# Kernel tuning notes

Measured on AMD Instinct MI355X. Metric: run time of the kernel, lower is better.

## Reference

```python
import jax, jax.numpy as jnp
import numpy as np

B, C, H = 8, 512, 2048
GROUPS = 32
EPS = 1e-6


def setup_inputs() -> dict:
    key = jax.random.key(0)
    ks = jax.random.split(key, 10)
    s = 1.0 / np.sqrt(C)
    return {
        "x": jax.random.normal(ks[0], (B, C, H), dtype=jnp.float32),
        "gamma": jnp.ones((C,), jnp.float32),
        "beta": jnp.zeros((C,), jnp.float32),
        "wq": jax.random.normal(ks[1], (C, C), jnp.float32) * s,
        "bq": jnp.zeros((C,), jnp.float32),
        "wk": jax.random.normal(ks[2], (C, C), jnp.float32) * s,
        "bk": jnp.zeros((C,), jnp.float32),
        "wv": jax.random.normal(ks[3], (C, C), jnp.float32) * s,
        "bv": jnp.zeros((C,), jnp.float32),
        "wp": jax.random.normal(ks[4], (C, C), jnp.float32) * s,
        "bp": jnp.zeros((C,), jnp.float32),
    }


def group_norm(x, gamma, beta):
    b, c, h = x.shape
    xr = x.reshape(b, GROUPS, c // GROUPS, h)
    mean = xr.mean(axis=(2, 3), keepdims=True)
    var = xr.var(axis=(2, 3), keepdims=True)
    xn = ((xr - mean) * jax.lax.rsqrt(var + EPS)).reshape(b, c, h)
    return xn * gamma[None, :, None] + beta[None, :, None]


def conv1x1(x, w, b):
    # 1x1 Conv1d == channel-mixing GEMM: [C_out,C_in] x [b,C_in,h]
    return jnp.einsum("oc,bch->boh", w, x) + b[None, :, None]


def reference(x, gamma, beta, wq, bq, wk, bk, wv, bv, wp, bp):
    b, c, h = x.shape
    hn = group_norm(x, gamma, beta)
    q = conv1x1(hn, wq, bq)  # [b,c,h]
    k = conv1x1(hn, wk, bk)
    v = conv1x1(hn, wv, bv)
    # scores w[b,i,j] = sum_c q[b,c,i] k[b,c,j] / sqrt(c)
    w = jnp.einsum("bci,bcj->bij", q, k) * (c ** -0.5)
    w = jax.nn.softmax(w, axis=2)
    # h_[b,c,i] = sum_j v[b,c,j] w[b,i,j]
    h_ = jnp.einsum("bcj,bij->bci", v, w)
    out = conv1x1(h_, wp, bp)
    return x + out
```

## Files before the change

### kernel.cpp

```cpp
#include <hip/hip_runtime.h>
#include <stdint.h>

typedef unsigned short u16;
typedef short s16x8 __attribute__((ext_vector_type(8)));
typedef float f32x4 __attribute__((ext_vector_type(4)));

#define BM 128
#define BN 128
#define BK 32
#define KPAD 40

#define WAITV(n) asm volatile("s_waitcnt vmcnt(" #n ")" ::: "memory")
#define BARR()   asm volatile("s_barrier" ::: "memory")
#define SB0()    __builtin_amdgcn_sched_barrier(0)

__device__ __forceinline__ float bf2f(u16 b) {
    union { unsigned int u; float f; } v; v.u = ((unsigned int)b) << 16; return v.f;
}
__device__ __forceinline__ u16 f2bf(float f) {
    union { float f; unsigned int u; } v; v.f = f;
    unsigned int u = v.u;
    u += 0x7fffu + ((u >> 16) & 1u);
    return (u16)(u >> 16);
}
__device__ __forceinline__ void async_cp16(const u16* g, u16* l) {
    __builtin_amdgcn_global_load_lds((const __attribute__((address_space(1))) void*)g,
                                     (__attribute__((address_space(3))) void*)l, 16, 0, 0);
}

__global__ __launch_bounds__(256) void gn_stats(const float* __restrict__ x,
                                                float* __restrict__ mean,
                                                float* __restrict__ rstd) {
    const int bg = blockIdx.x;
    const float* p = x + (long)bg * 16 * 2048;
    float s = 0.f, ss = 0.f;
    for (int it = 0; it < 32; it++) {
        const float4 v = *reinterpret_cast<const float4*>(p + ((it * 256 + threadIdx.x) << 2));
        s += v.x + v.y + v.z + v.w;
        ss += v.x * v.x + v.y * v.y + v.z * v.z + v.w * v.w;
    }
    const int lane = threadIdx.x & 63, wave = threadIdx.x >> 6;
#pragma unroll
    for (int o = 32; o > 0; o >>= 1) { s += __shfl_down(s, o, 64); ss += __shfl_down(ss, o, 64); }
    __shared__ float rb[8];
    if (lane == 0) { rb[wave] = s; rb[4 + wave] = ss; }
    __syncthreads();
    if (threadIdx.x == 0) {
        float S = rb[0] + rb[1] + rb[2] + rb[3];
        float SS = rb[4] + rb[5] + rb[6] + rb[7];
        float mu = S * (1.f / 32768.f);
        float var = SS * (1.f / 32768.f) - mu * mu;
        mean[bg] = mu;
        rstd[bg] = rsqrtf(var + 1e-6f);
    }
}

__global__ __launch_bounds__(256) void gn_apply_t(const float* __restrict__ x,
                                                  const float* __restrict__ gamma,
                                                  const float* __restrict__ beta,
                                                  const float* __restrict__ mean,
                                                  const float* __restrict__ rstd,
                                                  u16* __restrict__ hnT) {
    const int b = blockIdx.z, c0 = blockIdx.y * 64, h0 = blockIdx.x * 64;
    __shared__ __align__(16) u16 T[64][72];
    const int tid = threadIdx.x;
#pragma unroll
    for (int sidx = 0; sidx < 4; sidx++) {
        int ch = tid + sidx * 256;
        int cc = ch >> 4, h4 = (ch & 15) * 4;
        int c = c0 + cc;
        float mu = mean[b * 32 + (c >> 4)], rs = rstd[b * 32 + (c >> 4)];
        float ga = gamma[c], be = beta[c];
        const float4 v = *reinterpret_cast<const float4*>(x + ((long)b * 512 + c) * 2048 + h0 + h4);
        ushort4 pk;
        pk.x = f2bf((v.x - mu) * rs * ga + be);
        pk.y = f2bf((v.y - mu) * rs * ga + be);
        pk.z = f2bf((v.z - mu) * rs * ga + be);
        pk.w = f2bf((v.w - mu) * rs * ga + be);
        *reinterpret_cast<ushort4*>(&T[cc][h4]) = pk;
    }
    __syncthreads();
#pragma unroll
    for (int sidx = 0; sidx < 2; sidx++) {
        int ch = tid + sidx * 256;
        int hh = ch >> 3, c8 = (ch & 7) * 8;
        unsigned int o[4];
#pragma unroll
        for (int i = 0; i < 4; i++) {
            u16 lo = T[c8 + 2 * i][hh];
            u16 hi = T[c8 + 2 * i + 1][hh];
            o[i] = (unsigned int)lo | ((unsigned int)hi << 16);
        }
        *reinterpret_cast<uint4*>(hnT + ((long)b * 2048 + h0 + hh) * 512 + c0 + c8) =
            uint4{o[0], o[1], o[2], o[3]};
    }
}

__global__ __launch_bounds__(256) void w2bf(const float* __restrict__ a,
                                            const float* __restrict__ b,
                                            const float* __restrict__ c,
                                            u16* __restrict__ dst) {
    const float* s = (blockIdx.y == 0) ? a : (blockIdx.y == 1) ? b : c;
    const int i = (blockIdx.x * 256 + threadIdx.x) * 4;
    const float4 v = *reinterpret_cast<const float4*>(s + i);
    ushort4 p;
    p.x = f2bf(v.x); p.y = f2bf(v.y); p.z = f2bf(v.z); p.w = f2bf(v.w);
    *reinterpret_cast<ushort4*>(dst + (long)blockIdx.y * 262144 + i) = p;
}

__global__ __launch_bounds__(256) void softmax_rows(u16* __restrict__ S) {
    u16* p = S + (long)blockIdx.x * 2048;
    const int tid = threadIdx.x;
    uint4 v = *reinterpret_cast<const uint4*>(p + (tid << 3));
    unsigned int w[4] = {v.x, v.y, v.z, v.w};
    float f[8];
#pragma unroll
    for (int i = 0; i < 4; i++) {
        f[2 * i]     = bf2f((u16)(w[i] & 0xffffu));
        f[2 * i + 1] = bf2f((u16)(w[i] >> 16));
    }
    float m = f[0];
#pragma unroll
    for (int i = 1; i < 8; i++) m = fmaxf(m, f[i]);
    const int lane = tid & 63, wave = tid >> 6;
#pragma unroll
    for (int o = 32; o > 0; o >>= 1) m = fmaxf(m, __shfl_down(m, o, 64));
    __shared__ float rb[4];
    __shared__ float bc;
    if (lane == 0) rb[wave] = m;
    __syncthreads();
    if (tid == 0) bc = fmaxf(fmaxf(rb[0], rb[1]), fmaxf(rb[2], rb[3]));
    __syncthreads();
    m = bc;
    float s = 0.f;
#pragma unroll
    for (int i = 0; i < 8; i++) { f[i] = __expf(f[i] - m); s += f[i]; }
#pragma unroll
    for (int o = 32; o > 0; o >>= 1) s += __shfl_down(s, o, 64);
    __syncthreads();
    if (lane == 0) rb[wave] = s;
    __syncthreads();
    if (tid == 0) bc = 1.f / (rb[0] + rb[1] + rb[2] + rb[3]);
    __syncthreads();
    const float inv = bc;
#pragma unroll
    for (int i = 0; i < 4; i++)
        w[i] = (unsigned int)f2bf(f[2 * i] * inv) | ((unsigned int)f2bf(f[2 * i + 1] * inv) << 16);
    *reinterpret_cast<uint4*>(p + (tid << 3)) = uint4{w[0], w[1], w[2], w[3]};
}

__global__ __launch_bounds__(512, 1) void gemm256_s(const u16* __restrict__ Ag, long sA,
                                                    const u16* __restrict__ Bg, long sB,
                                                    u16* __restrict__ Og, long sO,
                                                    int K, int lda, int ldb, int ldo,
                                                    float scale) {
    const int bx = blockIdx.x;
    const int b = bx & 7, s = bx >> 3;
    const int ty = s & 7, tx = s >> 3;
    const int m0 = ty * 256, n0 = tx * 256;
    Ag += (long)b * sA;
    Bg += (long)b * sB;
    u16* O = Og + (long)b * sO;

    __shared__ __align__(16) u16 LA[2][2][128 * 64];
    __shared__ __align__(16) u16 LB[2][2][128 * 64];

    const int tid = threadIdx.x;
    const int lane = tid & 63, wave = tid >> 6;
    const int wm = wave >> 2, w4 = wave & 3;
    const int l15 = lane & 15, quad = lane >> 4;

    const int sw   = (l15 & 7) << 3;
    const int slt0 = ((quad << 3)) ^ sw;
    const int slt1 = (32 + (quad << 3)) ^ sw;
    const int arow_u = (wm * 64 + l15) * 64;
    const int brow_u = (w4 * 32 + l15) * 64;

    const int l8 = lane >> 3;
    const int lrow0 = wave * 8 + l8;
    const int sEl = (((lane & 7) ^ ((lane >> 3) & 7)) << 3);
    int pA[2], pB[2];
    pA[0] = (m0 + lrow0) * lda + sEl;
    pA[1] = (m0 + 64 + lrow0) * lda + sEl;
    {
        const int gb = (lrow0 >> 5) * 64 + (lrow0 & 31);
        pB[0] = (n0 + gb) * ldb + sEl;
        pB[1] = (n0 + gb + 32) * ldb + sEl;
    }
    const int jA = 128 * lda;
    const int jB = 128 * ldb;

    auto stageA = [&](int buf, int mh, int k0) {
        u16* d = &LA[buf][mh][wave * 512];
        async_cp16(Ag + pA[mh] + k0, d);
        async_cp16(Ag + pA[mh] + jA + k0, d + 4096);
    };
    auto stageB = [&](int buf, int nh, int k0) {
        u16* d = &LB[buf][nh][wave * 512];
        async_cp16(Bg + pB[nh] + k0, d);
        async_cp16(Bg + pB[nh] + jB + k0, d + 4096);
    };

    f32x4 acc[8][4];
#pragma unroll
    for (int i = 0; i < 8; i++)
#pragma unroll
        for (int j = 0; j < 4; j++) acc[i][j] = f32x4{0.f, 0.f, 0.f, 0.f};

    s16x8 fa[4][2], fblo[2][2], fbhi[2][2];

    const int NT = K >> 6;

    stageA(0, 0, 0);
    stageB(0, 0, 0);
    stageB(0, 1, 0);
    stageA(0, 1, 0);
    if (NT > 1) {
        stageA(1, 0, 64);
        stageB(1, 0, 64);
        stageB(1, 1, 64);
    }
    WAITV(8); SB0();
    BARR(); SB0();

    for (int t = 0; t < NT; t++) {
        const int buf = t & 1;
        const int k2 = (t + 2) << 6;
        {
            const u16* Ar = &LA[buf][0][0];
            const u16* Br = &LB[buf][0][0];
#pragma unroll
            for (int mf = 0; mf < 4; mf++)
#pragma unroll
                for (int ks = 0; ks < 2; ks++)
                    fa[mf][ks] = *reinterpret_cast<const s16x8*>(Ar + arow_u + mf * 1024 + (ks ? slt1 : slt0));
#pragma unroll
            for (int nf = 0; nf < 2; nf++)
#pragma unroll
                for (int ks = 0; ks < 2; ks++)
                    fblo[nf][ks] = *reinterpret_cast<const s16x8*>(Br + brow_u + nf * 1024 + (ks ? slt1 : slt0));
            if (t + 1 < NT) stageA(buf ^ 1, 1, (t + 1) << 6);
            if (t == NT - 1) { WAITV(2); } else { WAITV(8); }
            SB0();
            BARR(); SB0();
            __builtin_amdgcn_s_setprio(1);
#pragma unroll
            for (int mf = 0; mf < 4; mf++)
#pragma unroll
                for (int nf = 0; nf < 2; nf++)
#pragma unroll
                    for (int ks = 0; ks < 2; ks++)
                        acc[mf][nf] = __builtin_amdgcn_mfma_f32_16x16x32_bf16(fa[mf][ks], fblo[nf][ks], acc[mf][nf], 0, 0, 0);
            __builtin_amdgcn_s_setprio(0);
            BARR(); SB0();
        }
        {
            const u16* Br = &LB[buf][1][0];
#pragma unroll
            for (int nf = 0; nf < 2; nf++)
#pragma unroll
                for (int ks = 0; ks < 2; ks++)
                    fbhi[nf][ks] = *reinterpret_cast<const s16x8*>(Br + brow_u + nf * 1024 + (ks ? slt1 : slt0));
            if (t + 2 < NT) stageA(buf, 0, k2);
            if (t == NT - 1) { WAITV(0); } else { WAITV(8); }
            SB0();
            BARR(); SB0();
            __builtin_amdgcn_s_setprio(1);
#pragma unroll
            for (int mf = 0; mf < 4; mf++)
#pragma unroll
                for (int nf = 0; nf < 2; nf++)
#pragma unroll
                    for (int ks = 0; ks < 2; ks++)
                        acc[mf][2 + nf] = __builtin_amdgcn_mfma_f32_16x16x32_bf16(fa[mf][ks], fbhi[nf][ks], acc[mf][2 + nf], 0, 0, 0);
            __builtin_amdgcn_s_setprio(0);
            BARR(); SB0();
        }
        {
            const u16* Ar = &LA[buf][1][0];
#pragma unroll
            for (int mf = 0; mf < 4; mf++)
#pragma unroll
                for (int ks = 0; ks < 2; ks++)
                    fa[mf][ks] = *reinterpret_cast<const s16x8*>(Ar + arow_u + mf * 1024 + (ks ? slt1 : slt0));
            if (t + 2 < NT) stageB(buf, 0, k2);
            WAITV(8); SB0();
            BARR(); SB0();
            __builtin_amdgcn_s_setprio(1);
#pragma unroll
            for (int mf = 0; mf < 4; mf++)
#pragma unroll
                for (int nf = 0; nf < 2; nf++)
#pragma unroll
                    for (int ks = 0; ks < 2; ks++)
                        acc[4 + mf][2 + nf] = __builtin_amdgcn_mfma_f32_16x16x32_bf16(fa[mf][ks], fbhi[nf][ks], acc[4 + mf][2 + nf], 0, 0, 0);
            __builtin_amdgcn_s_setprio(0);
            BARR(); SB0();
        }
        {
            if (t + 2 < NT) stageB(buf, 1, k2);
            if (t == NT - 2) { WAITV(4); } else { WAITV(8); }
            SB0();
            BARR(); SB0();
            __builtin_amdgcn_s_setprio(1);
#pragma unroll
            for (int mf = 0; mf < 4; mf++)
#pragma unroll
                for (int nf = 0; nf < 2; nf++)
#pragma unroll
                    for (int ks = 0; ks < 2; ks++)
                        acc[4 + mf][nf] = __builtin_amdgcn_mfma_f32_16x16x32_bf16(fa[mf][ks], fblo[nf][ks], acc[4 + mf][nf], 0, 0, 0);
            __builtin_amdgcn_s_setprio(0);
            BARR(); SB0();
        }
    }

    const int orow = m0 + wm * 128 + quad * 4;
    const int ocol = n0 + w4 * 64 + l15;
#pragma unroll
    for (int mi = 0; mi < 8; mi++)
#pragma unroll
        for (int ni = 0; ni < 4; ni++) {
            const long rb = (long)(orow + mi * 16) * ldo + ocol + ni * 16;
#pragma unroll
            for (int r = 0; r < 4; r++)
                O[rb + (long)r * ldo] = f2bf(acc[mi][ni][r] * scale);
        }
}

template <int EPI>
__global__ __launch_bounds__(512, 1) void gemm256_pv(const u16* __restrict__ Ag, long sA,
                                                     const u16* __restrict__ Bg, long sB,
                                                     u16* __restrict__ Og, long sO,
                                                     int K, int lda, int ldb, int ldo,
                                                     float scale) {
    const int bx = blockIdx.x;
    const int b = bx & 7, s = bx >> 3;
    const int mt = s >> 2, nt = s & 3;
    const int m0 = mt * 256, n0 = nt * 128;
    Ag += (long)b * sA;
    Bg += (long)b * sB;
    u16* O = Og + (long)b * sO;

    __shared__ __align__(16) u16 LA[2][2][128 * 64];
    __shared__ __align__(16) u16 LB[2][2][64 * 64];

    const int tid = threadIdx.x;
    const int lane = tid & 63, wave = tid >> 6;
    const int wm = wave >> 1, wn = wave & 1;
    const int l15 = lane & 15, quad = lane >> 4;

    const int sw   = (l15 & 7) << 3;
    const int slt0 = ((quad << 3)) ^ sw;
    const int slt1 = (32 + (quad << 3)) ^ sw;

    const int r0 = tid >> 3;
    const int sEl = (((lane & 7) ^ ((lane >> 3) & 7)) << 3);
    const int gA = (r0 >> 5) * 64 + (r0 & 31);
    int pA[2], pB[2];
    pA[0] = (m0 + gA) * lda + sEl;
    pA[1] = (m0 + gA + 32) * lda + sEl;
    pB[0] = (n0 + gA) * ldb + sEl;
    pB[1] = (n0 + gA + 32) * ldb + sEl;
    const int jA = 128 * lda;

    auto stageA = [&](int buf, int mh, int k0) {
        u16* d = &LA[buf][mh][wave * 512];
        async_cp16(Ag + pA[mh] + k0, d);
        async_cp16(Ag + pA[mh] + jA + k0, d + 4096);
    };
    auto stageBB = [&](int buf, int k0) {
        async_cp16(Bg + pB[0] + k0, &LB[buf][0][wave * 512]);
        async_cp16(Bg + pB[1] + k0, &LB[buf][1][wave * 512]);
    };

    f32x4 acc[4][4];
#pragma unroll
    for (int i = 0; i < 4; i++)
#pragma unroll
        for (int j = 0; j < 4; j++) acc[i][j] = f32x4{0.f, 0.f, 0.f, 0.f};

    s16x8 fa[2][2], fblo[2][2], fbhi[2][2];

    const int arow_u = (wm * 32 + l15) * 64;
    const int brow_u = (wn * 32 + l15) * 64;

    const int NT = K >> 6;

    stageBB(0, 0);
    stageA(0, 0, 0);
    stageA(0, 1, 0);
    if (NT > 1) stageBB(1, 64);
    WAITV(4); SB0();
    BARR(); SB0();

    for (int t = 0; t < NT; t++) {
        const int buf = t & 1;
        const int k1 = (t + 1) << 6, k2 = (t + 2) << 6;
        {
            const u16* Ar = &LA[buf][0][0];
            const u16* Br = &LB[buf][0][0];
#pragma unroll
            for (int mf = 0; mf < 2; mf++)
#pragma unroll
                for (int ks = 0; ks < 2; ks++)
                    fa[mf][ks] = *reinterpret_cast<const s16x8*>(Ar + arow_u + mf * 1024 + (ks ? slt1 : slt0));
#pragma unroll
            for (int nf = 0; nf < 2; nf++)
#pragma unroll
                for (int ks = 0; ks < 2; ks++)
                    fblo[nf][ks] = *reinterpret_cast<const s16x8*>(Br + brow_u + nf * 1024 + (ks ? slt1 : slt0));
            if (t + 1 < NT) stageA(buf ^ 1, 0, k1);
            __builtin_amdgcn_s_setprio(1);
#pragma unroll
            for (int mf = 0; mf < 2; mf++)
#pragma unroll
                for (int nf = 0; nf < 2; nf++)
#pragma unroll
                    for (int ks = 0; ks < 2; ks++)
                        acc[mf][nf] = __builtin_amdgcn_mfma_f32_16x16x32_bf16(fa[mf][ks], fblo[nf][ks], acc[mf][nf], 0, 0, 0);
            __builtin_amdgcn_s_setprio(0);
            if (t == NT - 1) { WAITV(0); } else { WAITV(4); }
            SB0();
            BARR(); SB0();
        }
        {
            const u16* Br = &LB[buf][1][0];
#pragma unroll
            for (int nf = 0; nf < 2; nf++)
#pragma unroll
                for (int ks = 0; ks < 2; ks++)
                    fbhi[nf][ks] = *reinterpret_cast<const s16x8*>(Br + brow_u + nf * 1024 + (ks ? slt1 : slt0));
            if (t + 1 < NT) stageA(buf ^ 1, 1, k1);
            __builtin_amdgcn_s_setprio(1);
#pragma unroll
            for (int mf = 0; mf < 2; mf++)
#pragma unroll
                for (int nf = 0; nf < 2; nf++)
#pragma unroll
                    for (int ks = 0; ks < 2; ks++)
                        acc[mf][2 + nf] = __builtin_amdgcn_mfma_f32_16x16x32_bf16(fa[mf][ks], fbhi[nf][ks], acc[mf][2 + nf], 0, 0, 0);
            __builtin_amdgcn_s_setprio(0);
            BARR(); SB0();
        }
        {
            const u16* Ar = &LA[buf][1][0];
#pragma unroll
            for (int mf = 0; mf < 2; mf++)
#pragma unroll
                for (int ks = 0; ks < 2; ks++)
                    fa[mf][ks] = *reinterpret_cast<const s16x8*>(Ar + arow_u + mf * 1024 + (ks ? slt1 : slt0));
            if (t + 2 < NT) stageBB(buf, k2);
            __builtin_amdgcn_s_setprio(1);
#pragma unroll
            for (int mf = 0; mf < 2; mf++)
#pragma unroll
                for (int nf = 0; nf < 2; nf++)
#pragma unroll
                    for (int ks = 0; ks < 2; ks++)
                        acc[2 + mf][2 + nf] = __builtin_amdgcn_mfma_f32_16x16x32_bf16(fa[mf][ks], fbhi[nf][ks], acc[2 + mf][2 + nf], 0, 0, 0);
            __builtin_amdgcn_s_setprio(0);
            BARR(); SB0();
        }
        {
            __builtin_amdgcn_s_setprio(1);
#pragma unroll
            for (int mf = 0; mf < 2; mf++)
#pragma unroll
                for (int nf = 0; nf < 2; nf++)
#pragma unroll
                    for (int ks = 0; ks < 2; ks++)
                        acc[2 + mf][nf] = __builtin_amdgcn_mfma_f32_16x16x32_bf16(fa[mf][ks], fblo[nf][ks], acc[2 + mf][nf], 0, 0, 0);
            __builtin_amdgcn_s_setprio(0);
            if (t == NT - 2) { WAITV(2); } else if (t < NT - 2) { WAITV(4); }
            SB0();
            BARR(); SB0();
        }
    }

    const int orow = m0 + wm * 64 + quad * 4;
    const int ocol = n0 + wn * 64 + l15;
#pragma unroll
    for (int mi = 0; mi < 4; mi++)
#pragma unroll
        for (int ni = 0; ni < 4; ni++) {
            const long rb = (long)(orow + mi * 16) * ldo + ocol + ni * 16;
#pragma unroll
            for (int r = 0; r < 4; r++)
                O[rb + (long)r * ldo] = f2bf(acc[mi][ni][r] * scale);
        }
}

template <int EPI, int SWIZ>
__global__ __launch_bounds__(256) void gemm_tn_a(const u16* __restrict__ Ag, long sA,
                                                 const u16* __restrict__ Bg, long sB,
                                                 const float* __restrict__ bias,
                                                 const float* __restrict__ Xg, long sX,
                                                 void* __restrict__ Ogv, long sO,
                                                 int K, int lda, int ldb, int ldo,
                                                 float scale) {
    const int b = blockIdx.z;
    Ag += (long)b * sA;
    Bg += (long)b * sB;
    int tx, ty;
    if (SWIZ == 1) {
        const int xcd = blockIdx.x & 7, s = blockIdx.x >> 3;
        ty = xcd + 8 * (s >> 2);
        tx = s & 3;
    } else if (SWIZ == 2) {
        const int xcd = blockIdx.x & 7, s = blockIdx.x >> 3;
        ty = (xcd & 3) * 4 + (s & 3);
        tx = (xcd >> 2) * 8 + (s >> 2);
    } else {
        tx = blockIdx.x; ty = blockIdx.y;
    }
    const int m0 = ty * BM;
    const int n0 = tx * BN;

    __shared__ __align__(16) u16 As[3][BM * BK];
    __shared__ __align__(16) u16 Bs[3][BN * BK];

    const int tid = threadIdx.x;
    const int wave = tid >> 6;
    const int lane = tid & 63;
    const int quad = lane >> 4;
    const int l16 = lane & 15;
    const int wm = (wave >> 1) * 64;
    const int wn = (wave & 1) * 64;
    const int rl = lane >> 2;
    const int cl = (lane & 3) * 8;

    f32x4 acc[4][4];
#pragma unroll
    for (int i = 0; i < 4; i++)
#pragma unroll
        for (int j = 0; j < 4; j++) acc[i][j] = f32x4{0.f, 0.f, 0.f, 0.f};

    auto stage = [&](int buf, int k0) {
#pragma unroll
        for (int j = 0; j < 2; j++) {
            const int rbase = wave * 32 + j * 16;
            async_cp16(Ag + (long)(m0 + rbase + rl) * lda + k0 + cl, &As[buf][rbase * BK]);
            async_cp16(Bg + (long)(n0 + rbase + rl) * ldb + k0 + cl, &Bs[buf][rbase * BK]);
        }
    };
    auto compute = [&](int buf) {
        s16x8 af[4], bfr[4];
#pragma unroll
        for (int i = 0; i < 4; i++)
            af[i] = *reinterpret_cast<const s16x8*>(&As[buf][(wm + i * 16 + l16) * BK + quad * 8]);
#pragma unroll
        for (int j = 0; j < 4; j++)
            bfr[j] = *reinterpret_cast<const s16x8*>(&Bs[buf][(wn + j * 16 + l16) * BK + quad * 8]);
#pragma unroll
        for (int i = 0; i < 4; i++)
#pragma unroll
            for (int j = 0; j < 4; j++)
                acc[i][j] = __builtin_amdgcn_mfma_f32_16x16x32_bf16(af[i], bfr[j], acc[i][j], 0, 0, 0);
    };

    const int nsteps = K / BK;
    stage(0, 0);
    stage(1, BK);
    int t = 0;
    for (; t < nsteps - 1; t++) {
        asm volatile("s_waitcnt vmcnt(4)" ::: "memory");
        asm volatile("s_barrier" ::: "memory");
        if (t + 2 < nsteps) stage((t + 2) % 3, (t + 2) * BK);
        compute(t % 3);
    }
    asm volatile("s_waitcnt vmcnt(0)" ::: "memory");
    asm volatile("s_barrier" ::: "memory");
    compute(t % 3);

#pragma unroll
    for (int i = 0; i < 4; i++) {
        const int mb = m0 + wm + i * 16 + quad * 4;
#pragma unroll
        for (int j = 0; j < 4; j++) {
            const int n = n0 + wn + j * 16 + l16;
            if (EPI == 0) {
                u16* O = (u16*)Ogv + (long)b * sO;
#pragma unroll
                for (int r = 0; r < 4; r++) {
                    float vv = acc[i][j][r] * scale;
                    if (bias) vv += bias[mb + r];
                    O[(long)(mb + r) * ldo + n] = f2bf(vv);
                }
            } else if (EPI == 1) {
                u16* O = (u16*)Ogv + (long)b * sO;
                ushort4 pk;
                pk.x = f2bf(acc[i][j][0] + bias[mb + 0]);
                pk.y = f2bf(acc[i][j][1] + bias[mb + 1]);
                pk.z = f2bf(acc[i][j][2] + bias[mb + 2]);
                pk.w = f2bf(acc[i][j][3] + bias[mb + 3]);
                *reinterpret_cast<ushort4*>(&O[(long)n * ldo + mb]) = pk;
            } else {
                float* O = (float*)Ogv + (long)b * sO;
                const float* X = Xg + (long)b * sX;
                const float bn = bias[n];
                const float4 xv = *reinterpret_cast<const float4*>(&X[(long)n * ldo + mb]);
                float4 pk;
                pk.x = acc[i][j][0] + bn + xv.x;
                pk.y = acc[i][j][1] + bn + xv.y;
                pk.z = acc[i][j][2] + bn + xv.z;
                pk.w = acc[i][j][3] + bn + xv.w;
                *reinterpret_cast<float4*>(&O[(long)n * ldo + mb]) = pk;
            }
        }
    }
}

__global__ __launch_bounds__(256) void qkv_a(const u16* __restrict__ wb3,
                                             const u16* __restrict__ hnT,
                                             const float* __restrict__ bq,
                                             const float* __restrict__ bk,
                                             const float* __restrict__ bv,
                                             u16* __restrict__ qT, u16* __restrict__ kT,
                                             u16* __restrict__ vv) {
    const long HC = 1048576;
    const int b = blockIdx.z;
    const int xcd = blockIdx.x & 7, s = blockIdx.x >> 3;
    const int hi = (s >= 12) ? 1 : 0;
    const int yy = s - hi * 12;
    const int x = xcd + 8 * hi;
    const int which = yy >> 2;
    const int my = yy & 3;
    const u16* Ag = wb3 + which * 262144;
    const u16* Bg = hnT + (long)b * HC;
    const int m0 = my * BM;
    const int n0 = x * BN;

    __shared__ __align__(16) u16 As[3][BM * BK];
    __shared__ __align__(16) u16 Bs[3][BN * BK];

    const int tid = threadIdx.x;
    const int wave = tid >> 6;
    const int lane = tid & 63;
    const int quad = lane >> 4;
    const int l16 = lane & 15;
    const int wm = (wave >> 1) * 64;
    const int wn = (wave & 1) * 64;
    const int rl = lane >> 2;
    const int cl = (lane & 3) * 8;

    f32x4 acc[4][4];
#pragma unroll
    for (int i = 0; i < 4; i++)
#pragma unroll
        for (int j = 0; j < 4; j++) acc[i][j] = f32x4{0.f, 0.f, 0.f, 0.f};

    auto stage = [&](int buf, int k0) {
#pragma unroll
        for (int j = 0; j < 2; j++) {
            const int rbase = wave * 32 + j * 16;
            async_cp16(Ag + (long)(m0 + rbase + rl) * 512 + k0 + cl, &As[buf][rbase * BK]);
            async_cp16(Bg + (long)(n0 + rbase + rl) * 512 + k0 + cl, &Bs[buf][rbase * BK]);
        }
    };
    auto compute = [&](int buf) {
        s16x8 af[4], bfr[4];
#pragma unroll
        for (int i = 0; i < 4; i++)
            af[i] = *reinterpret_cast<const s16x8*>(&As[buf][(wm + i * 16 + l16) * BK + quad * 8]);
#pragma unroll
        for (int j = 0; j < 4; j++)
            bfr[j] = *reinterpret_cast<const s16x8*>(&Bs[buf][(wn + j * 16 + l16) * BK + quad * 8]);
#pragma unroll
        for (int i = 0; i < 4; i++)
#pragma unroll
            for (int j = 0; j < 4; j++)
                acc[i][j] = __builtin_amdgcn_mfma_f32_16x16x32_bf16(af[i], bfr[j], acc[i][j], 0, 0, 0);
    };

    const int nsteps = 512 / BK;
    stage(0, 0);
    stage(1, BK);
    int t = 0;
    for (; t < nsteps - 1; t++) {
        asm volatile("s_waitcnt vmcnt(4)" ::: "memory");
        asm volatile("s_barrier" ::: "memory");
        if (t + 2 < nsteps) stage((t + 2) % 3, (t + 2) * BK);
        compute(t % 3);
    }
    asm volatile("s_waitcnt vmcnt(0)" ::: "memory");
    asm volatile("s_barrier" ::: "memory");
    compute(t % 3);

    if (which == 2) {
        u16* O = vv + (long)b * HC;
#pragma unroll
        for (int i = 0; i < 4; i++) {
            const int mb = m0 + wm + i * 16 + quad * 4;
#pragma unroll
            for (int j = 0; j < 4; j++) {
                const int n = n0 + wn + j * 16 + l16;
#pragma unroll
                for (int r = 0; r < 4; r++)
                    O[(long)(mb + r) * 2048 + n] = f2bf(acc[i][j][r] + bv[mb + r]);
            }
        }
    } else {
        const float* bias = which ? bk : bq;
        u16* O = (which ? kT : qT) + (long)b * HC;
#pragma unroll
        for (int i = 0; i < 4; i++) {
            const int mb = m0 + wm + i * 16 + quad * 4;
#pragma unroll
            for (int j = 0; j < 4; j++) {
                const int n = n0 + wn + j * 16 + l16;
                ushort4 pk;
                pk.x = f2bf(acc[i][j][0] + bias[mb + 0]);
                pk.y = f2bf(acc[i][j][1] + bias[mb + 1]);
                pk.z = f2bf(acc[i][j][2] + bias[mb + 2]);
                pk.w = f2bf(acc[i][j][3] + bias[mb + 3]);
                *reinterpret_cast<ushort4*>(&O[(long)n * 512 + mb]) = pk;
            }
        }
    }
}

template <int F32>
__device__ __forceinline__ void stage_tile(const char* G, int ld, int r0, int k0,
                                           u16* __restrict__ lds, int tid) {
    if (F32) {
        const float* g = (const float*)G;
#pragma unroll
        for (int s = 0; s < 4; s++) {
            const int c = tid + s * 256;
            const int row = c >> 3, col = (c & 7) * 4;
            const float4 v = *reinterpret_cast<const float4*>(g + (long)(r0 + row) * ld + k0 + col);
            ushort4 pk;
            pk.x = f2bf(v.x); pk.y = f2bf(v.y); pk.z = f2bf(v.z); pk.w = f2bf(v.w);
            *reinterpret_cast<ushort4*>(&lds[row * KPAD + col]) = pk;
        }
    } else {
        const u16* g = (const u16*)G;
#pragma unroll
        for (int s = 0; s < 2; s++) {
            const int c = tid + s * 256;
            const int row = c >> 2, col = (c & 3) * 8;
            const uint4 v = *reinterpret_cast<const uint4*>(g + (long)(r0 + row) * ld + k0 + col);
            *reinterpret_cast<uint4*>(&lds[row * KPAD + col]) = v;
        }
    }
}

template <int EPI, int AF32, int BF32>
__global__ __launch_bounds__(256) void gemm_tn(const void* __restrict__ Agv, long sA,
                                               const void* __restrict__ Bgv, long sB,
                                               const float* __restrict__ bias,
                                               const float* __restrict__ Xg, long sX,
                                               void* __restrict__ Ogv, long sO,
                                               int K, int lda, int ldb, int ldo,
                                               float scale) {
    const int b = blockIdx.z;
    const char* A8 = (const char*)Agv + (long)b * sA * (AF32 ? 4 : 2);
    const char* B8 = (const char*)Bgv + (long)b * sB * (BF32 ? 4 : 2);
    const int m0 = blockIdx.y * BM;
    const int n0 = blockIdx.x * BN;

    __shared__ __align__(16) u16 As[BM * KPAD];
    __shared__ __align__(16) u16 Bs[BN * KPAD];

    const int tid = threadIdx.x;
    const int wave = tid >> 6;
    const int lane = tid & 63;
    const int quad = lane >> 4;
    const int l16 = lane & 15;
    const int wm = (wave >> 1) * 64;
    const int wn = (wave & 1) * 64;

    f32x4 acc[4][4];
#pragma unroll
    for (int i = 0; i < 4; i++)
#pragma unroll
        for (int j = 0; j < 4; j++) acc[i][j] = f32x4{0.f, 0.f, 0.f, 0.f};

    for (int k0 = 0; k0 < K; k0 += BK) {
        __syncthreads();
        stage_tile<AF32>(A8, lda, m0, k0, As, tid);
        stage_tile<BF32>(B8, ldb, n0, k0, Bs, tid);
        __syncthreads();
        s16x8 af[4], bfr[4];
#pragma unroll
        for (int i = 0; i < 4; i++)
            af[i] = *reinterpret_cast<const s16x8*>(&As[(wm + i * 16 + l16) * KPAD + quad * 8]);
#pragma unroll
        for (int j = 0; j < 4; j++)
            bfr[j] = *reinterpret_cast<const s16x8*>(&Bs[(wn + j * 16 + l16) * KPAD + quad * 8]);
#pragma unroll
        for (int i = 0; i < 4; i++)
#pragma unroll
            for (int j = 0; j < 4; j++)
                acc[i][j] = __builtin_amdgcn_mfma_f32_16x16x32_bf16(af[i], bfr[j], acc[i][j], 0, 0, 0);
    }

#pragma unroll
    for (int i = 0; i < 4; i++) {
        const int mb = m0 + wm + i * 16 + quad * 4;
#pragma unroll
        for (int j = 0; j < 4; j++) {
            const int n = n0 + wn + j * 16 + l16;
            if (EPI == 0) {
                u16* O = (u16*)Ogv + (long)b * sO;
#pragma unroll
                for (int r = 0; r < 4; r++) {
                    float vv = acc[i][j][r] * scale;
                    if (bias) vv += bias[mb + r];
                    O[(long)(mb + r) * ldo + n] = f2bf(vv);
                }
            } else if (EPI == 1) {
                u16* O = (u16*)Ogv + (long)b * sO;
                ushort4 pk;
                pk.x = f2bf(acc[i][j][0] + bias[mb + 0]);
                pk.y = f2bf(acc[i][j][1] + bias[mb + 1]);
                pk.z = f2bf(acc[i][j][2] + bias[mb + 2]);
                pk.w = f2bf(acc[i][j][3] + bias[mb + 3]);
                *reinterpret_cast<ushort4*>(&O[(long)n * ldo + mb]) = pk;
            } else {
                float* O = (float*)Ogv + (long)b * sO;
                const float* X = Xg + (long)b * sX;
                const float bn = bias[n];
                const float4 xv = *reinterpret_cast<const float4*>(&X[(long)n * ldo + mb]);
                float4 pk;
                pk.x = acc[i][j][0] + bn + xv.x;
                pk.y = acc[i][j][1] + bn + xv.y;
                pk.z = acc[i][j][2] + bn + xv.z;
                pk.w = acc[i][j][3] + bn + xv.w;
                *reinterpret_cast<float4*>(&O[(long)n * ldo + mb]) = pk;
            }
        }
    }
}

extern "C" void kernel_launch(void* const* d_in, const int* in_sizes, int n_in,
                              void* d_out, int out_size, void* d_ws, size_t ws_size,
                              hipStream_t stream) {
    const float* x     = (const float*)d_in[0];
    const float* gamma = (const float*)d_in[1];
    const float* beta  = (const float*)d_in[2];
    const float* wq    = (const float*)d_in[3];
    const float* bq    = (const float*)d_in[4];
    const float* wk    = (const float*)d_in[5];
    const float* bk    = (const float*)d_in[6];
    const float* wv    = (const float*)d_in[7];
    const float* bv    = (const float*)d_in[8];
    const float* wp    = (const float*)d_in[9];
    const float* bp    = (const float*)d_in[10];
    float* out = (float*)d_out;

    const long HC = (long)2048 * 512;
    const long HH = (long)2048 * 2048;
    const long WSZ = 512 * 512;
    const float scl = 0.044194173824159216f;

    char* ws = (char*)d_ws;
    float* meanb = (float*)ws;
    float* rstdb = (float*)(ws + 1024);
    u16* base = (u16*)(ws + 4096);

    const size_t FULL_NEED   = 4096 + 2 * (size_t)(24 * HC + 8 * HH);
    const size_t MED_NEED    = 4096 + 2 * (size_t)(32 * HC + HH);
    const size_t SMALL_NEED  = 4096 + 2 * (size_t)(4 * HC + HH);
    const size_t CHUNK512    = 4096 + 2 * (size_t)(4 * HC + 512 * 2048);

    gn_stats<<<256, 256, 0, stream>>>(x, meanb, rstdb);

    if (ws_size >= FULL_NEED) {
        u16* qT  = base;
        u16* kT  = qT + 8 * HC;
        u16* vv  = kT + 8 * HC;
        u16* Sb  = vv + 8 * HC;
        u16* hnT = Sb;
        u16* wb3 = Sb + 8 * HH - 3 * WSZ;
        u16* hT  = qT;
        u16* wpb = vv;

        w2bf<<<dim3(256, 3), 256, 0, stream>>>(wq, wk, wv, wb3);
        gn_apply_t<<<dim3(32, 8, 8), 256, 0, stream>>>(x, gamma, beta, meanb, rstdb, hnT);
        qkv_a<<<dim3(192, 1, 8), 256, 0, stream>>>(wb3, hnT, bq, bk, bv, qT, kT, vv);
        gemm256_s<<<dim3(512), 512, 0, stream>>>(qT, HC, kT, HC, Sb, HH,
                                                 512, 512, 512, 2048, scl);
        softmax_rows<<<16384, 256, 0, stream>>>(Sb);
        gemm256_pv<0><<<dim3(256), 512, 0, stream>>>(Sb, HH, vv, HC, hT, HC,
                                                     2048, 2048, 2048, 512, 1.f);
        w2bf<<<dim3(256, 1), 256, 0, stream>>>(wp, wp, wp, wpb);
        gemm_tn_a<2, 1><<<dim3(64, 1, 8), 256, 0, stream>>>(hT, HC, wpb, 0, bp, x, HC,
                                                            out, HC, 512, 512, 512, 2048, 1.f);
    } else if (ws_size >= MED_NEED) {
        u16* hnT = base;
        u16* qT  = hnT + 8 * HC;
        u16* kT  = qT + 8 * HC;
        u16* vv  = kT + 8 * HC;
        u16* Sb  = vv + 8 * HC;
        u16* hT  = hnT;
        gn_apply_t<<<dim3(32, 8, 8), 256, 0, stream>>>(x, gamma, beta, meanb, rstdb, hnT);
        gemm_tn<1, 1, 0><<<dim3(16, 4, 8), 256, 0, stream>>>(wq, 0, hnT, HC, bq, nullptr, 0,
                                                             qT, HC, 512, 512, 512, 512, 1.f);
        gemm_tn<1, 1, 0><<<dim3(16, 4, 8), 256, 0, stream>>>(wk, 0, hnT, HC, bk, nullptr, 0,
                                                             kT, HC, 512, 512, 512, 512, 1.f);
        gemm_tn<0, 1, 0><<<dim3(16, 4, 8), 256, 0, stream>>>(wv, 0, hnT, HC, bv, nullptr, 0,
                                                             vv, HC, 512, 512, 512, 2048, 1.f);
        for (int b = 0; b < 8; b++) {
            gemm_tn<0, 0, 0><<<dim3(16, 16, 1), 256, 0, stream>>>(qT + b * HC, 0, kT + b * HC, 0,
                                                                  nullptr, nullptr, 0, Sb, 0,
                                                                  512, 512, 512, 2048, scl);
            softmax_rows<<<2048, 256, 0, stream>>>(Sb);
            gemm_tn<0, 0, 0><<<dim3(4, 16, 1), 256, 0, stream>>>(Sb, 0, vv + b * HC, 0,
                                                                 nullptr, nullptr, 0, hT + b * HC, 0,
                                                                 2048, 2048, 2048, 512, 1.f);
        }
        gemm_tn<2, 0, 1><<<dim3(4, 16, 8), 256, 0, stream>>>(hT, HC, wp, 0, bp, x, HC,
                                                             out, HC, 512, 512, 512, 2048, 1.f);
    } else {
        const int CH = (ws_size >= SMALL_NEED) ? 2048 : ((ws_size >= CHUNK512) ? 512 : 128);
        u16* hn = base;
        u16* q  = hn + HC;
        u16* k  = q + HC;
        u16* v  = k + HC;
        u16* Sc = v + HC;
        u16* hT = hn;
        for (int b = 0; b < 8; b++) {
            const float* xb = x + (long)b * HC;
            gn_apply_t<<<dim3(32, 8, 1), 256, 0, stream>>>(xb, gamma, beta,
                                                           meanb + b * 32, rstdb + b * 32, hn);
            gemm_tn<1, 1, 0><<<dim3(16, 4, 1), 256, 0, stream>>>(wq, 0, hn, 0, bq, nullptr, 0,
                                                                 q, 0, 512, 512, 512, 512, 1.f);
            gemm_tn<1, 1, 0><<<dim3(16, 4, 1), 256, 0, stream>>>(wk, 0, hn, 0, bk, nullptr, 0,
                                                                 k, 0, 512, 512, 512, 512, 1.f);
            gemm_tn<0, 1, 0><<<dim3(16, 4, 1), 256, 0, stream>>>(wv, 0, hn, 0, bv, nullptr, 0,
                                                                 v, 0, 512, 512, 512, 2048, 1.f);
            for (int i0 = 0; i0 < 2048; i0 += CH) {
                gemm_tn<0, 0, 0><<<dim3(16, CH / 128, 1), 256, 0, stream>>>(
                    q + (long)i0 * 512, 0, k, 0, nullptr, nullptr, 0, Sc, 0,
                    512, 512, 512, 2048, scl);
                softmax_rows<<<CH, 256, 0, stream>>>(Sc);
                gemm_tn<0, 0, 0><<<dim3(4, CH / 128, 1), 256, 0, stream>>>(
                    Sc, 0, v, 0, nullptr, nullptr, 0, hT + (long)i0 * 512, 0,
                    2048, 2048, 2048, 512, 1.f);
            }
            gemm_tn<2, 0, 1><<<dim3(4, 16, 1), 256, 0, stream>>>(hT, 0, wp, 0, bp, xb, 0,
                                                                 out + (long)b * HC, 0,
                                                                 512, 512, 512, 2048, 1.f);
        }
    }
}
```

Measured before the change: 284.7 us.

## Replace QKV projection kernel with 256x128-tile, 512-thread swizzled-LDS pipelined GEMM

Replaces the 128x128-tile, 256-thread QKV projection kernel with a 256x128-tile kernel using 8 waves, BK=64, XOR-swizzled LDS and a four-phase interleaved prefetch schedule borrowed from the scores GEMM. The grid is flattened with batch in the low bits so blocks of the same batch spread across XCDs. The aim is better data reuse per block and fewer LDS bank conflicts, with loads overlapping MFMA work. In exchange, fewer blocks launch (768 of 512 threads) and the larger tile raises register and LDS pressure.

```diff
diff --git a/kernel.cpp b/kernel.cpp
--- a/kernel.cpp
+++ b/kernel.cpp
@@ -489,6 +489,195 @@
             for (int r = 0; r < 4; r++)
                 O[rb + (long)r * ldo] = f2bf(acc[mi][ni][r] * scale);
         }
+}
+
+__global__ __launch_bounds__(512, 1) void qkv256(const u16* __restrict__ wb3,
+                                                 const u16* __restrict__ hnT,
+                                                 const float* __restrict__ bq,
+                                                 const float* __restrict__ bk,
+                                                 const float* __restrict__ bv,
+                                                 u16* __restrict__ qT, u16* __restrict__ kT,
+                                                 u16* __restrict__ vv) {
+    const long HC = 1048576;
+    const int bx = blockIdx.x;
+    const int b = bx & 7, s = bx >> 3;
+    const int nt = s & 15, mt = s >> 4;
+    const int m0 = mt * 256, n0 = nt * 128;
+    const u16* Ag = wb3;
+    const u16* Bg = hnT + (long)b * HC;
+    const int which = mt >> 1;
+    const float* bias = (which == 0) ? bq : (which == 1) ? bk : bv;
+    const int mbase = m0 & 511;
+    const int lda = 512, ldb = 512;
+
+    __shared__ __align__(16) u16 LA[2][2][128 * 64];
+    __shared__ __align__(16) u16 LB[2][2][64 * 64];
+
+    const int tid = threadIdx.x;
+    const int lane = tid & 63, wave = tid >> 6;
+    const int wm = wave >> 1, wn = wave & 1;
+    const int l15 = lane & 15, quad = lane >> 4;
+
+    const int sw   = (l15 & 7) << 3;
+    const int slt0 = ((quad << 3)) ^ sw;
+    const int slt1 = (32 + (quad << 3)) ^ sw;
+
+    const int r0 = tid >> 3;
+    const int sEl = (((lane & 7) ^ ((lane >> 3) & 7)) << 3);
+    const int gA = (r0 >> 5) * 64 + (r0 & 31);
+    int pA[2], pB[2];
+    pA[0] = (m0 + gA) * lda + sEl;
+    pA[1] = (m0 + gA + 32) * lda + sEl;
+    pB[0] = (n0 + gA) * ldb + sEl;
+    pB[1] = (n0 + gA + 32) * ldb + sEl;
+    const int jA = 128 * lda;
+
+    auto stageA = [&](int buf, int mh, int k0) {
+        u16* d = &LA[buf][mh][wave * 512];
+        async_cp16(Ag + pA[mh] + k0, d);
+        async_cp16(Ag + pA[mh] + jA + k0, d + 4096);
+    };
+    auto stageBB = [&](int buf, int k0) {
+        async_cp16(Bg + pB[0] + k0, &LB[buf][0][wave * 512]);
+        async_cp16(Bg + pB[1] + k0, &LB[buf][1][wave * 512]);
+    };
+
+    f32x4 acc[4][4];
+#pragma unroll
+    for (int i = 0; i < 4; i++)
+#pragma unroll
+        for (int j = 0; j < 4; j++) acc[i][j] = f32x4{0.f, 0.f, 0.f, 0.f};
+
+    s16x8 fa[2][2], fblo[2][2], fbhi[2][2];
+
+    const int arow_u = (wm * 32 + l15) * 64;
+    const int brow_u = (wn * 32 + l15) * 64;
+
+    const int NT = 8;
+
+    stageBB(0, 0);
+    stageA(0, 0, 0);
+    stageA(0, 1, 0);
+    stageBB(1, 64);
+    WAITV(4); SB0();
+    BARR(); SB0();
+
+    for (int t = 0; t < NT; t++) {
+        const int buf = t & 1;
+        const int k1 = (t + 1) << 6, k2 = (t + 2) << 6;
+        {
+            const u16* Ar = &LA[buf][0][0];
+            const u16* Br = &LB[buf][0][0];
+#pragma unroll
+            for (int mf = 0; mf < 2; mf++)
+#pragma unroll
+                for (int ks = 0; ks < 2; ks++)
+                    fa[mf][ks] = *reinterpret_cast<const s16x8*>(Ar + arow_u + mf * 1024 + (ks ? slt1 : slt0));
+#pragma unroll
+            for (int nf = 0; nf < 2; nf++)
+#pragma unroll
+                for (int ks = 0; ks < 2; ks++)
+                    fblo[nf][ks] = *reinterpret_cast<const s16x8*>(Br + brow_u + nf * 1024 + (ks ? slt1 : slt0));
+            if (t + 1 < NT) stageA(buf ^ 1, 0, k1);
+            __builtin_amdgcn_s_setprio(1);
+#pragma unroll
+            for (int mf = 0; mf < 2; mf++)
+#pragma unroll
+                for (int nf = 0; nf < 2; nf++)
+#pragma unroll
+                    for (int ks = 0; ks < 2; ks++)
+                        acc[mf][nf] = __builtin_amdgcn_mfma_f32_16x16x32_bf16(fa[mf][ks], fblo[nf][ks], acc[mf][nf], 0, 0, 0);
+            __builtin_amdgcn_s_setprio(0);
+            if (t == NT - 1) { WAITV(0); } else { WAITV(4); }
+            SB0();
+            BARR(); SB0();
+        }
+        {
+            const u16* Br = &LB[buf][1][0];
+#pragma unroll
+            for (int nf = 0; nf < 2; nf++)
+#pragma unroll
+                for (int ks = 0; ks < 2; ks++)
+                    fbhi[nf][ks] = *reinterpret_cast<const s16x8*>(Br + brow_u + nf * 1024 + (ks ? slt1 : slt0));
+            if (t + 1 < NT) stageA(buf ^ 1, 1, k1);
+            __builtin_amdgcn_s_setprio(1);
+#pragma unroll
+            for (int mf = 0; mf < 2; mf++)
+#pragma unroll
+                for (int nf = 0; nf < 2; nf++)
+#pragma unroll
+                    for (int ks = 0; ks < 2; ks++)
+                        acc[mf][2 + nf] = __builtin_amdgcn_mfma_f32_16x16x32_bf16(fa[mf][ks], fbhi[nf][ks], acc[mf][2 + nf], 0, 0, 0);
+            __builtin_amdgcn_s_setprio(0);
+            BARR(); SB0();
+        }
+        {
+            const u16* Ar = &LA[buf][1][0];
+#pragma unroll
+            for (int mf = 0; mf < 2; mf++)
+#pragma unroll
+                for (int ks = 0; ks < 2; ks++)
+                    fa[mf][ks] = *reinterpret_cast<const s16x8*>(Ar + arow_u + mf * 1024 + (ks ? slt1 : slt0));
+            if (t + 2 < NT) stageBB(buf, k2);
+            __builtin_amdgcn_s_setprio(1);
+#pragma unroll
+            for (int mf = 0; mf < 2; mf++)
+#pragma unroll
+                for (int nf = 0; nf < 2; nf++)
+#pragma unroll
+                    for (int ks = 0; ks < 2; ks++)
+                        acc[2 + mf][2 + nf] = __builtin_amdgcn_mfma_f32_16x16x32_bf16(fa[mf][ks], fbhi[nf][ks], acc[2 + mf][2 + nf], 0, 0, 0);
+            __builtin_amdgcn_s_setprio(0);
+            BARR(); SB0();
+        }
+        {
+            __builtin_amdgcn_s_setprio(1);
+#pragma unroll
+            for (int mf = 0; mf < 2; mf++)
+#pragma unroll
+                for (int nf = 0; nf < 2; nf++)
+#pragma unroll
+                    for (int ks = 0; ks < 2; ks++)
+                        acc[2 + mf][nf] = __builtin_amdgcn_mfma_f32_16x16x32_bf16(fa[mf][ks], fblo[nf][ks], acc[2 + mf][nf], 0, 0, 0);
+            __builtin_amdgcn_s_setprio(0);
+            if (t == NT - 2) { WAITV(2); } else if (t < NT - 2) { WAITV(4); }
+            SB0();
+            BARR(); SB0();
+        }
+    }
+
+    const int orow = mbase + wm * 64 + quad * 4;
+    const int ocol = n0 + wn * 64 + l15;
+    if (which < 2) {
+        u16* O = (which ? kT : qT) + (long)b * HC;
+#pragma unroll
+        for (int mi = 0; mi < 4; mi++) {
+            const int rowb = orow + mi * 16;
+#pragma unroll
+            for (int ni = 0; ni < 4; ni++) {
+                const int n = ocol + ni * 16;
+                ushort4 pk;
+                pk.x = f2bf(acc[mi][ni][0] + bias[rowb + 0]);
+                pk.y = f2bf(acc[mi][ni][1] + bias[rowb + 1]);
+                pk.z = f2bf(acc[mi][ni][2] + bias[rowb + 2]);
+                pk.w = f2bf(acc[mi][ni][3] + bias[rowb + 3]);
+                *reinterpret_cast<ushort4*>(&O[(long)n * 512 + rowb]) = pk;
+            }
+        }
+    } else {
+        u16* O = vv + (long)b * HC;
+#pragma unroll
+        for (int mi = 0; mi < 4; mi++) {
+            const int rowb = orow + mi * 16;
+#pragma unroll
+            for (int ni = 0; ni < 4; ni++) {
+                const int n = ocol + ni * 16;
+#pragma unroll
+                for (int r = 0; r < 4; r++)
+                    O[(long)(rowb + r) * 2048 + n] = f2bf(acc[mi][ni][r] + bias[rowb + r]);
+            }
+        }
+    }
 }
 
 template <int EPI, int SWIZ>
@@ -611,115 +800,6 @@
     }
 }
 
-__global__ __launch_bounds__(256) void qkv_a(const u16* __restrict__ wb3,
-                                             const u16* __restrict__ hnT,
-                                             const float* __restrict__ bq,
-                                             const float* __restrict__ bk,
-                                             const float* __restrict__ bv,
-                                             u16* __restrict__ qT, u16* __restrict__ kT,
-                                             u16* __restrict__ vv) {
-    const long HC = 1048576;
-    const int b = blockIdx.z;
-    const int xcd = blockIdx.x & 7, s = blockIdx.x >> 3;
-    const int hi = (s >= 12) ? 1 : 0;
-    const int yy = s - hi * 12;
-    const int x = xcd + 8 * hi;
-    const int which = yy >> 2;
-    const int my = yy & 3;
-    const u16* Ag = wb3 + which * 262144;
-    const u16* Bg = hnT + (long)b * HC;
-    const int m0 = my * BM;
-    const int n0 = x * BN;
-
-    __shared__ __align__(16) u16 As[3][BM * BK];
-    __shared__ __align__(16) u16 Bs[3][BN * BK];
-
-    const int tid = threadIdx.x;
-    const int wave = tid >> 6;
-    const int lane = tid & 63;
-    const int quad = lane >> 4;
-    const int l16 = lane & 15;
-    const int wm = (wave >> 1) * 64;
-    const int wn = (wave & 1) * 64;
-    const int rl = lane >> 2;
-    const int cl = (lane & 3) * 8;
-
-    f32x4 acc[4][4];
-#pragma unroll
-    for (int i = 0; i < 4; i++)
-#pragma unroll
-        for (int j = 0; j < 4; j++) acc[i][j] = f32x4{0.f, 0.f, 0.f, 0.f};
-
-    auto stage = [&](int buf, int k0) {
-#pragma unroll
-        for (int j = 0; j < 2; j++) {
-            const int rbase = wave * 32 + j * 16;
-            async_cp16(Ag + (long)(m0 + rbase + rl) * 512 + k0 + cl, &As[buf][rbase * BK]);
-            async_cp16(Bg + (long)(n0 + rbase + rl) * 512 + k0 + cl, &Bs[buf][rbase * BK]);
-        }
-    };
-    auto compute = [&](int buf) {
-        s16x8 af[4], bfr[4];
-#pragma unroll
-        for (int i = 0; i < 4; i++)
-            af[i] = *reinterpret_cast<const s16x8*>(&As[buf][(wm + i * 16 + l16) * BK + quad * 8]);
-#pragma unroll
-        for (int j = 0; j < 4; j++)
-            bfr[j] = *reinterpret_cast<const s16x8*>(&Bs[buf][(wn + j * 16 + l16) * BK + quad * 8]);
-#pragma unroll
-        for (int i = 0; i < 4; i++)
-#pragma unroll
-            for (int j = 0; j < 4; j++)
-                acc[i][j] = __builtin_amdgcn_mfma_f32_16x16x32_bf16(af[i], bfr[j], acc[i][j], 0, 0, 0);
-    };
-
-    const int nsteps = 512 / BK;
-    stage(0, 0);
-    stage(1, BK);
-    int t = 0;
-    for (; t < nsteps - 1; t++) {
-        asm volatile("s_waitcnt vmcnt(4)" ::: "memory");
-        asm volatile("s_barrier" ::: "memory");
-        if (t + 2 < nsteps) stage((t + 2) % 3, (t + 2) * BK);
-        compute(t % 3);
-    }
-    asm volatile("s_waitcnt vmcnt(0)" ::: "memory");
-    asm volatile("s_barrier" ::: "memory");
-    compute(t % 3);
-
-    if (which == 2) {
-        u16* O = vv + (long)b * HC;
-#pragma unroll
-        for (int i = 0; i < 4; i++) {
-            const int mb = m0 + wm + i * 16 + quad * 4;
-#pragma unroll
-            for (int j = 0; j < 4; j++) {
-                const int n = n0 + wn + j * 16 + l16;
-#pragma unroll
-                for (int r = 0; r < 4; r++)
-                    O[(long)(mb + r) * 2048 + n] = f2bf(acc[i][j][r] + bv[mb + r]);
-            }
-        }
-    } else {
-        const float* bias = which ? bk : bq;
-        u16* O = (which ? kT : qT) + (long)b * HC;
-#pragma unroll
-        for (int i = 0; i < 4; i++) {
-            const int mb = m0 + wm + i * 16 + quad * 4;
-#pragma unroll
-            for (int j = 0; j < 4; j++) {
-                const int n = n0 + wn + j * 16 + l16;
-                ushort4 pk;
-                pk.x = f2bf(acc[i][j][0] + bias[mb + 0]);
-                pk.y = f2bf(acc[i][j][1] + bias[mb + 1]);
-                pk.z = f2bf(acc[i][j][2] + bias[mb + 2]);
-                pk.w = f2bf(acc[i][j][3] + bias[mb + 3]);
-                *reinterpret_cast<ushort4*>(&O[(long)n * 512 + mb]) = pk;
-            }
-        }
-    }
-}
-
 template <int F32>
 __device__ __forceinline__ void stage_tile(const char* G, int ld, int r0, int k0,
                                            u16* __restrict__ lds, int tid) {
@@ -879,7 +959,7 @@
 
         w2bf<<<dim3(256, 3), 256, 0, stream>>>(wq, wk, wv, wb3);
         gn_apply_t<<<dim3(32, 8, 8), 256, 0, stream>>>(x, gamma, beta, meanb, rstdb, hnT);
-        qkv_a<<<dim3(192, 1, 8), 256, 0, stream>>>(wb3, hnT, bq, bk, bv, qT, kT, vv);
+        qkv256<<<dim3(768), 512, 0, stream>>>(wb3, hnT, bq, bk, bv, qT, kT, vv);
         gemm256_s<<<dim3(512), 512, 0, stream>>>(qT, HC, kT, HC, Sb, HH,
                                                  512, 512, 512, 2048, scl);
         softmax_rows<<<16384, 256, 0, stream>>>(Sb);
```

Result: faster. 274.7 us (-3.5%).
